# Optimization experiments

Hardware: AMD Instinct MI355X
Metric: run time of the kernel (lower is better)

Reference implementation:

```python
import jax, jax.numpy as jnp
import numpy as np

N_COARSE = 12500
N_FINE = 50000
MIN_BASIS = 16  # (min(L_in, L_out) + 1) ** 2 with L_in = L_out = 3


def setup_inputs() -> dict:
    key = jax.random.key(0)
    ks = jax.random.split(key, 8)
    return {
        "last_inv": jax.random.normal(ks[0], (N_COARSE, 256), dtype=jnp.float32),
        "cur_inv": jax.random.normal(ks[1], (N_FINE, 256), dtype=jnp.float32),
        "last_equ": jax.random.normal(ks[2], (N_COARSE, 16, 256), dtype=jnp.float32),
        "cur_equ": jax.random.normal(ks[3], (N_FINE, 16, 256), dtype=jnp.float32),
        "upsampling": jax.random.randint(ks[4], (N_FINE,), 0, N_COARSE, dtype=jnp.int32),
        # Linear weights stored as [in, out] (torch weight is [out, in]; x @ W.T == x @ W_in_out)
        "W_last_equ": jax.random.normal(ks[5], (256, 256), dtype=jnp.float32) * 0.02,
        "W_cur_equ": jax.random.normal(ks[6], (256, 256), dtype=jnp.float32) * 0.02,
        "W_mlp": jax.random.normal(ks[7], (768, 512), dtype=jnp.float32) * 0.02,
    }


def reference(last_inv, cur_inv, last_equ, cur_equ, upsampling, W_last_equ, W_cur_equ, W_mlp):
    # nearest_upsample: gather coarse rows up to fine resolution
    li = jnp.take(last_inv, upsampling, axis=0)                 # [N_fine, 256]
    le = jnp.take(last_equ, upsampling, axis=0)[:, :MIN_BASIS]  # [N_fine, 16, 256]
    le = jnp.einsum('nbc,cd->nbd', le, W_last_equ)              # fc_last_equ (no bias)
    ce = jnp.einsum('nbc,cd->nbd', cur_equ[:, :MIN_BASIS], W_cur_equ)  # fc_cur_equ
    equ = (ce * le).mean(axis=1)                                # [N_fine, 256]
    com = jnp.concatenate([li, cur_inv, equ], axis=-1)          # [N_fine, 768]
    return com @ W_mlp                                          # LastUnaryBlock: Linear, no bias
```

## Files before the change

kernel.cpp:

```cpp
#include <hip/hip_runtime.h>
#include <hip/hip_bf16.h>

#define N_COARSE 12500
#define N_FINE   50000

typedef __bf16 bf16x8 __attribute__((ext_vector_type(8)));
typedef __bf16 bf16x4 __attribute__((ext_vector_type(4)));
typedef float  f32x4  __attribute__((ext_vector_type(4)));


__device__ __forceinline__ bf16x8 cvt8(f32x4 x, f32x4 y) {
    bf16x8 r;
    r[0] = (__bf16)x[0]; r[1] = (__bf16)x[1]; r[2] = (__bf16)x[2]; r[3] = (__bf16)x[3];
    r[4] = (__bf16)y[0]; r[5] = (__bf16)y[1]; r[6] = (__bf16)y[2]; r[7] = (__bf16)y[3];
    return r;
}

__device__ __forceinline__ void lds_barrier() {
    asm volatile("s_waitcnt lgkmcnt(0)" ::: "memory");
    __builtin_amdgcn_s_barrier();
}

__device__ __forceinline__ void gl_lds16(const float* g, float* l) {
    __builtin_amdgcn_global_load_lds(
        (const __attribute__((address_space(1))) void*)g,
        (__attribute__((address_space(3))) void*)l, 16, 0, 0);
}

__device__ __forceinline__ int swz(int row, int byte) { return byte ^ ((row & 7) << 4); }
__device__ __forceinline__ void st_a(__bf16* lds, int row, int cs, bf16x8 v) {
    *(bf16x8*)((char*)lds + swz(row, row * 512 + cs * 16)) = v;
}
__device__ __forceinline__ bf16x8 ld_a(const __bf16* lds, int row, int ka) {
    return *(const bf16x8*)((const char*)lds + swz(row, row * 512 + ka * 2));
}

template<int NT>
__device__ __forceinline__ void stage_f32(const float* __restrict__ A, long row0,
                                          __bf16* lds, int tid, long maxrow) {
    const int r0 = tid >> 5, cs = tid & 31;
    constexpr int RPI = NT / 32;
    #pragma unroll
    for (int i = 0; i < 64 / RPI; ++i) {
        int row = r0 + i * RPI;
        long gr = row0 + row; if (gr > maxrow) gr = maxrow;
        const float* p = A + gr * 256 + cs * 8;
        f32x4 x = *(const f32x4*)p, y = *(const f32x4*)(p + 4);
        st_a(lds, row, cs, cvt8(x, y));
    }
}

__device__ __forceinline__ void mfma_tile(const __bf16* lds, const bf16x8* __restrict__ packB,
                                          int N, int c0, int ksb,
                                          f32x4 (&acc)[4][4], int lane) {
    const int g = lane >> 4, r15 = lane & 15;
    #pragma unroll
    for (int ks = 0; ks < 8; ++ks) {
        bf16x8 a[4];
        #pragma unroll
        for (int rt = 0; rt < 4; ++rt)
            a[rt] = ld_a(lds, rt * 16 + r15, ks * 32 + g * 8);
        const size_t kb = (size_t)((ksb + ks) * 4 + g) * N;
        #pragma unroll
        for (int ct = 0; ct < 4; ++ct) {
            bf16x8 b = packB[kb + c0 + ct * 16 + r15];
            #pragma unroll
            for (int rt = 0; rt < 4; ++rt)
                acc[rt][ct] = __builtin_amdgcn_mfma_f32_16x16x32_bf16(a[rt], b, acc[rt][ct], 0, 0, 0);
        }
    }
}

__global__ __launch_bounds__(256) void k_prep(
    const float* __restrict__ W_le, const float* __restrict__ W_ce,
    const float* __restrict__ W_mlp, const float* __restrict__ last_inv,
    __bf16* __restrict__ packLE, __bf16* __restrict__ packCE,
    __bf16* __restrict__ packM, __bf16* __restrict__ li_bf)
{
    const int b = blockIdx.x, tid = threadIdx.x;
    if (b < 256) {
        int idx = b * 256 + tid, k = idx >> 8, n = idx & 255;
        packLE[(((size_t)(k >> 3) << 8) + n) * 8 + (k & 7)] = (__bf16)W_le[idx];
    } else if (b < 512) {
        int idx = (b - 256) * 256 + tid, k = idx >> 8, n = idx & 255;
        packCE[(((size_t)(k >> 3) << 8) + n) * 8 + (k & 7)] = (__bf16)W_ce[idx];
    } else if (b < 2048) {
        int idx = (b - 512) * 256 + tid, k = idx >> 9, n = idx & 511;
        packM[(((size_t)(k >> 3) << 9) + n) * 8 + (k & 7)] = (__bf16)W_mlp[idx];
    } else {
        int i = (b - 2048) * 256 + tid;
        f32x4 v = ((const f32x4*)last_inv)[i];
        bf16x4 o;
        o[0] = (__bf16)v[0]; o[1] = (__bf16)v[1]; o[2] = (__bf16)v[2]; o[3] = (__bf16)v[3];
        ((bf16x4*)li_bf)[i] = o;
    }
}

__global__ __launch_bounds__(256) void k_coarse_equ(
    const float* __restrict__ last_equ, const bf16x8* __restrict__ packW,
    __bf16* __restrict__ LEp)
{
    __shared__ __attribute__((aligned(16))) float Af[2][32 * 256];
    const int tid = threadIdx.x, lane = tid & 63, wid = tid >> 6;
    const int g = lane >> 4, r15 = lane & 15;
    const int NT = N_COARSE * 16 / 32;
    const int per = (NT + gridDim.x - 1) / gridDim.x;
    const int tb = blockIdx.x * per;
    const int te = min(tb + per, NT);
    if (tb >= te) return;

    const int lhalf = (lane & 1) << 2;

    {
        const float* rb = last_equ + (size_t)tb * 32 * 256;
        #pragma unroll
        for (int i = 0; i < 8; ++i) {
            int row = wid * 8 + i;
            gl_lds16(rb + (size_t)row * 256 + ((((lane >> 1) ^ (row & 7)) << 3) + lhalf),
                     &Af[tb & 1][row * 256]);
        }
    }

    for (int t = tb; t < te; ++t) {
        asm volatile("s_waitcnt vmcnt(0)" ::: "memory");
        __builtin_amdgcn_s_barrier();

        if (t + 1 < te) {
            const float* rb = last_equ + (size_t)(t + 1) * 32 * 256;
            #pragma unroll
            for (int i = 0; i < 8; ++i) {
                int row = wid * 8 + i;
                gl_lds16(rb + (size_t)row * 256 + ((((lane >> 1) ^ (row & 7)) << 3) + lhalf),
                         &Af[(t + 1) & 1][row * 256]);
            }
        }

        const float* B = Af[t & 1];
        f32x4 acc[2][4] = {};
        #pragma unroll
        for (int ks = 0; ks < 8; ++ks) {
            bf16x8 a[2];
            #pragma unroll
            for (int rt = 0; rt < 2; ++rt) {
                int r = rt * 16 + r15;
                const float* p = B + r * 256 + (((4 * ks + g) ^ (r & 7)) << 3);
                a[rt] = cvt8(*(const f32x4*)p, *(const f32x4*)(p + 4));
            }
            const size_t kb = (size_t)(ks * 4 + g) * 256;
            #pragma unroll
            for (int ct = 0; ct < 4; ++ct) {
                bf16x8 b = packW[kb + wid * 64 + ct * 16 + r15];
                #pragma unroll
                for (int rt = 0; rt < 2; ++rt)
                    acc[rt][ct] = __builtin_amdgcn_mfma_f32_16x16x32_bf16(a[rt], b, acc[rt][ct], 0, 0, 0);
            }
        }

        #pragma unroll
        for (int rt = 0; rt < 2; ++rt) {
            int coarse = t * 2 + rt;
            #pragma unroll
            for (int ct = 0; ct < 4; ++ct) {
                int cg = wid * 4 + ct;
                bf16x4 v;
                v[0] = (__bf16)acc[rt][ct][0]; v[1] = (__bf16)acc[rt][ct][1];
                v[2] = (__bf16)acc[rt][ct][2]; v[3] = (__bf16)acc[rt][ct][3];
                *(bf16x4*)(LEp + ((size_t)(coarse * 16 + cg) * 64 + lane) * 4) = v;
            }
        }
    }
}

__global__ __launch_bounds__(256) void k_fine_equ(
    const float* __restrict__ cur_equ, const bf16x8* __restrict__ packW,
    const __bf16* __restrict__ LEp, const int* __restrict__ up,
    __bf16* __restrict__ equ)
{
    __shared__ __attribute__((aligned(16))) float Af[2][32 * 256];
    const int tid = threadIdx.x, lane = tid & 63, wid = tid >> 6;
    const int g = lane >> 4, r15 = lane & 15;
    const int NT = N_FINE / 2;
    const int per = (NT + gridDim.x - 1) / gridDim.x;
    const int tb = blockIdx.x * per;
    const int te = min(tb + per, NT);
    if (tb >= te) return;

    const int lhalf = (lane & 1) << 2;

    {
        const float* rb = cur_equ + (size_t)tb * 32 * 256;
        #pragma unroll
        for (int i = 0; i < 8; ++i) {
            int row = wid * 8 + i;
            gl_lds16(rb + (size_t)row * 256 + ((((lane >> 1) ^ (row & 7)) << 3) + lhalf),
                     &Af[tb & 1][row * 256]);
        }
    }

    for (int t = tb; t < te; ++t) {
        asm volatile("s_waitcnt vmcnt(0)" ::: "memory");
        __builtin_amdgcn_s_barrier();

        if (t + 1 < te) {
            const float* rb = cur_equ + (size_t)(t + 1) * 32 * 256;
            #pragma unroll
            for (int i = 0; i < 8; ++i) {
                int row = wid * 8 + i;
                gl_lds16(rb + (size_t)row * 256 + ((((lane >> 1) ^ (row & 7)) << 3) + lhalf),
                         &Af[(t + 1) & 1][row * 256]);
            }
        }

        const float* B = Af[t & 1];
        f32x4 acc[2][4] = {};
        #pragma unroll
        for (int ks = 0; ks < 8; ++ks) {
            bf16x8 a[2];
            #pragma unroll
            for (int rt = 0; rt < 2; ++rt) {
                int r = rt * 16 + r15;
                const float* p = B + r * 256 + (((4 * ks + g) ^ (r & 7)) << 3);
                a[rt] = cvt8(*(const f32x4*)p, *(const f32x4*)(p + 4));
            }
            const size_t kb = (size_t)(ks * 4 + g) * 256;
            #pragma unroll
            for (int ct = 0; ct < 4; ++ct) {
                bf16x8 b = packW[kb + wid * 64 + ct * 16 + r15];
                #pragma unroll
                for (int rt = 0; rt < 2; ++rt)
                    acc[rt][ct] = __builtin_amdgcn_mfma_f32_16x16x32_bf16(a[rt], b, acc[rt][ct], 0, 0, 0);
            }
        }

        const int n0 = t * 2;
        const int cu0 = up[n0], cu1 = up[n0 + 1];
        bf16x4 le[2][4];
        #pragma unroll
        for (int ct = 0; ct < 4; ++ct) {
            le[0][ct] = *(const bf16x4*)(LEp + ((size_t)(cu0 * 16 + wid * 4 + ct) * 64 + lane) * 4);
            le[1][ct] = *(const bf16x4*)(LEp + ((size_t)(cu1 * 16 + wid * 4 + ct) * 64 + lane) * 4);
        }
        #pragma unroll
        for (int rt = 0; rt < 2; ++rt) {
            #pragma unroll
            for (int ct = 0; ct < 4; ++ct) {
                float s = acc[rt][ct][0] * (float)le[rt][ct][0]
                        + acc[rt][ct][1] * (float)le[rt][ct][1]
                        + acc[rt][ct][2] * (float)le[rt][ct][2]
                        + acc[rt][ct][3] * (float)le[rt][ct][3];
                s += __shfl_xor(s, 16, 64);
                s += __shfl_xor(s, 32, 64);
                if (lane < 16)
                    equ[(size_t)(n0 + rt) * 256 + wid * 64 + ct * 16 + lane] =
                        (__bf16)(s * 0.0625f);
            }
        }
    }
}

__global__ __launch_bounds__(512) void k_out(
    const __bf16* __restrict__ li_bf, const float* __restrict__ cur_inv,
    const __bf16* __restrict__ equ, const bf16x8* __restrict__ packW,
    const int* __restrict__ up, float* __restrict__ out)
{
    __shared__ __attribute__((aligned(16))) __bf16 As[64 * 256];
    const int tid = threadIdx.x, lane = tid & 63, wid = tid >> 6;
    const int row0 = blockIdx.x * 64;
    const int c0 = wid * 64;
    const int r0 = tid >> 5, cs = tid & 31;
    f32x4 acc[4][4] = {};

    #pragma unroll
    for (int i = 0; i < 4; ++i) {
        int row = r0 + i * 16;
        int gr = row0 + row; if (gr > N_FINE - 1) gr = N_FINE - 1;
        st_a(As, row, cs, *(const bf16x8*)(li_bf + (size_t)up[gr] * 256 + cs * 8));
    }
    lds_barrier();
    mfma_tile(As, packW, 512, c0, 0, acc, lane);
    lds_barrier();

    stage_f32<512>(cur_inv, row0, As, tid, N_FINE - 1);
    lds_barrier();
    mfma_tile(As, packW, 512, c0, 8, acc, lane);
    lds_barrier();

    #pragma unroll
    for (int i = 0; i < 4; ++i) {
        int row = r0 + i * 16;
        int gr = row0 + row; if (gr > N_FINE - 1) gr = N_FINE - 1;
        st_a(As, row, cs, *(const bf16x8*)(equ + (size_t)gr * 256 + cs * 8));
    }
    lds_barrier();
    mfma_tile(As, packW, 512, c0, 16, acc, lane);

    const int g = lane >> 4, r15 = lane & 15;
    #pragma unroll
    for (int rt = 0; rt < 4; ++rt)
        #pragma unroll
        for (int j = 0; j < 4; ++j) {
            int r = row0 + rt * 16 + g * 4 + j;
            if (r < N_FINE)
                #pragma unroll
                for (int ct = 0; ct < 4; ++ct)
                    out[(size_t)r * 512 + c0 + ct * 16 + r15] = acc[rt][ct][j];
        }
}

extern "C" void kernel_launch(void* const* d_in, const int* in_sizes, int n_in,
                              void* d_out, int out_size, void* d_ws, size_t ws_size,
                              hipStream_t stream) {
    const float* last_inv = (const float*)d_in[0];
    const float* cur_inv  = (const float*)d_in[1];
    const float* last_equ = (const float*)d_in[2];
    const float* cur_equ  = (const float*)d_in[3];
    const int*   up       = (const int*)d_in[4];
    const float* W_le     = (const float*)d_in[5];
    const float* W_ce     = (const float*)d_in[6];
    const float* W_mlp    = (const float*)d_in[7];
    float* out = (float*)d_out;

    char* w = (char*)d_ws;
    __bf16* LEp    = (__bf16*)w;  w += (size_t)N_COARSE * 16 * 256 * 2;
    __bf16* equ    = (__bf16*)w;  w += (size_t)N_FINE * 256 * 2;
    __bf16* li_bf  = (__bf16*)w;  w += (size_t)N_COARSE * 256 * 2;
    __bf16* packLE = (__bf16*)w;  w += (size_t)256 * 256 * 2;
    __bf16* packCE = (__bf16*)w;  w += (size_t)256 * 256 * 2;
    __bf16* packM  = (__bf16*)w;  w += (size_t)768 * 512 * 2;

    k_prep<<<2048 + 3125, 256, 0, stream>>>(
        W_le, W_ce, W_mlp, last_inv, packLE, packCE, packM, li_bf);

    k_coarse_equ<<<512, 256, 0, stream>>>(
        last_equ, (const bf16x8*)packLE, LEp);

    k_fine_equ<<<512, 256, 0, stream>>>(
        cur_equ, (const bf16x8*)packCE, LEp, up, equ);

    k_out<<<(N_FINE + 63) / 64, 512, 0, stream>>>(
        li_bf, cur_inv, equ, (const bf16x8*)packM, up, out);
}
```

Before: 483.4 us.

## Double-buffer k_out A-tiles with async global-to-LDS loads and pre-convert cur_inv

Moves the fp32-to-bf16 conversion of cur_inv into the prep kernel, so the output GEMM reads a bf16 copy. k_out now stages each A segment straight into LDS with global_load_lds into two buffers, so the next segment's load overlaps MFMA on the current one. The aim is to hide load latency in k_out and drop the register round-trip. The cost is an extra full pass writing and reading a 25.6MB bf16 copy of cur_inv, plus double the LDS per block, which may lower occupancy.

```diff
diff --git a/kernel.cpp b/kernel.cpp
--- a/kernel.cpp
+++ b/kernel.cpp
@@ -16,38 +16,15 @@
     return r;
 }
 
-__device__ __forceinline__ void lds_barrier() {
-    asm volatile("s_waitcnt lgkmcnt(0)" ::: "memory");
-    __builtin_amdgcn_s_barrier();
-}
-
-__device__ __forceinline__ void gl_lds16(const float* g, float* l) {
+__device__ __forceinline__ void gl_lds16(const void* g, void* l) {
     __builtin_amdgcn_global_load_lds(
         (const __attribute__((address_space(1))) void*)g,
         (__attribute__((address_space(3))) void*)l, 16, 0, 0);
 }
 
 __device__ __forceinline__ int swz(int row, int byte) { return byte ^ ((row & 7) << 4); }
-__device__ __forceinline__ void st_a(__bf16* lds, int row, int cs, bf16x8 v) {
-    *(bf16x8*)((char*)lds + swz(row, row * 512 + cs * 16)) = v;
-}
 __device__ __forceinline__ bf16x8 ld_a(const __bf16* lds, int row, int ka) {
     return *(const bf16x8*)((const char*)lds + swz(row, row * 512 + ka * 2));
-}
-
-template<int NT>
-__device__ __forceinline__ void stage_f32(const float* __restrict__ A, long row0,
-                                          __bf16* lds, int tid, long maxrow) {
-    const int r0 = tid >> 5, cs = tid & 31;
-    constexpr int RPI = NT / 32;
-    #pragma unroll
-    for (int i = 0; i < 64 / RPI; ++i) {
-        int row = r0 + i * RPI;
-        long gr = row0 + row; if (gr > maxrow) gr = maxrow;
-        const float* p = A + gr * 256 + cs * 8;
-        f32x4 x = *(const f32x4*)p, y = *(const f32x4*)(p + 4);
-        st_a(lds, row, cs, cvt8(x, y));
-    }
 }
 
 __device__ __forceinline__ void mfma_tile(const __bf16* lds, const bf16x8* __restrict__ packB,
@@ -74,8 +51,10 @@
 __global__ __launch_bounds__(256) void k_prep(
     const float* __restrict__ W_le, const float* __restrict__ W_ce,
     const float* __restrict__ W_mlp, const float* __restrict__ last_inv,
+    const float* __restrict__ cur_inv,
     __bf16* __restrict__ packLE, __bf16* __restrict__ packCE,
-    __bf16* __restrict__ packM, __bf16* __restrict__ li_bf)
+    __bf16* __restrict__ packM, __bf16* __restrict__ li_bf,
+    __bf16* __restrict__ ci_bf)
 {
     const int b = blockIdx.x, tid = threadIdx.x;
     if (b < 256) {
@@ -87,12 +66,18 @@
     } else if (b < 2048) {
         int idx = (b - 512) * 256 + tid, k = idx >> 9, n = idx & 511;
         packM[(((size_t)(k >> 3) << 9) + n) * 8 + (k & 7)] = (__bf16)W_mlp[idx];
-    } else {
+    } else if (b < 2048 + 3125) {
         int i = (b - 2048) * 256 + tid;
         f32x4 v = ((const f32x4*)last_inv)[i];
         bf16x4 o;
         o[0] = (__bf16)v[0]; o[1] = (__bf16)v[1]; o[2] = (__bf16)v[2]; o[3] = (__bf16)v[3];
         ((bf16x4*)li_bf)[i] = o;
+    } else {
+        int i = (b - 2048 - 3125) * 256 + tid;
+        f32x4 v = ((const f32x4*)cur_inv)[i];
+        bf16x4 o;
+        o[0] = (__bf16)v[0]; o[1] = (__bf16)v[1]; o[2] = (__bf16)v[2]; o[3] = (__bf16)v[3];
+        ((bf16x4*)ci_bf)[i] = o;
     }
 }
 
@@ -110,7 +95,6 @@
     if (tb >= te) return;
 
     const int lhalf = (lane & 1) << 2;
-
     {
         const float* rb = last_equ + (size_t)tb * 32 * 256;
         #pragma unroll
@@ -186,7 +170,6 @@
     if (tb >= te) return;
 
     const int lhalf = (lane & 1) << 2;
-
     {
         const float* rb = cur_equ + (size_t)tb * 32 * 256;
         #pragma unroll
@@ -259,40 +242,54 @@
 }
 
 __global__ __launch_bounds__(512) void k_out(
-    const __bf16* __restrict__ li_bf, const float* __restrict__ cur_inv,
+    const __bf16* __restrict__ li_bf, const __bf16* __restrict__ ci_bf,
     const __bf16* __restrict__ equ, const bf16x8* __restrict__ packW,
     const int* __restrict__ up, float* __restrict__ out)
 {
-    __shared__ __attribute__((aligned(16))) __bf16 As[64 * 256];
-    const int tid = threadIdx.x, lane = tid & 63, wid = tid >> 6;
+    __shared__ __attribute__((aligned(16))) __bf16 Ab[2][64 * 256];
+    const int tid = threadIdx.x, lane = tid & 63;
+    const int c0 = (tid >> 6) * 64;
     const int row0 = blockIdx.x * 64;
-    const int c0 = wid * 64;
-    const int r0 = tid >> 5, cs = tid & 31;
+    const int wbase = (tid >> 6) * 2;
+
+    #pragma unroll
+    for (int i = 0; i < 4; ++i) {
+        int rw = (tid >> 5) + i * 16;
+        int gr = row0 + rw; if (gr > N_FINE - 1) gr = N_FINE - 1;
+        int gran = (tid & 31) ^ (rw & 7);
+        gl_lds16(li_bf + (size_t)up[gr] * 256 + gran * 8,
+                 &Ab[0][(wbase + i * 16) * 256]);
+    }
+
     f32x4 acc[4][4] = {};
 
+    asm volatile("s_waitcnt vmcnt(0)" ::: "memory");
+    __builtin_amdgcn_s_barrier();
     #pragma unroll
     for (int i = 0; i < 4; ++i) {
-        int row = r0 + i * 16;
-        int gr = row0 + row; if (gr > N_FINE - 1) gr = N_FINE - 1;
-        st_a(As, row, cs, *(const bf16x8*)(li_bf + (size_t)up[gr] * 256 + cs * 8));
-    }
-    lds_barrier();
-    mfma_tile(As, packW, 512, c0, 0, acc, lane);
-    lds_barrier();
-
-    stage_f32<512>(cur_inv, row0, As, tid, N_FINE - 1);
-    lds_barrier();
-    mfma_tile(As, packW, 512, c0, 8, acc, lane);
-    lds_barrier();
-
+        int rw = (tid >> 5) + i * 16;
+        int gr = row0 + rw; if (gr > N_FINE - 1) gr = N_FINE - 1;
+        int gran = (tid & 31) ^ (rw & 7);
+        gl_lds16(ci_bf + (size_t)gr * 256 + gran * 8,
+                 &Ab[1][(wbase + i * 16) * 256]);
+    }
+    mfma_tile(Ab[0], packW, 512, c0, 0, acc, lane);
+
+    asm volatile("s_waitcnt vmcnt(0)" ::: "memory");
+    __builtin_amdgcn_s_barrier();
     #pragma unroll
     for (int i = 0; i < 4; ++i) {
-        int row = r0 + i * 16;
-        int gr = row0 + row; if (gr > N_FINE - 1) gr = N_FINE - 1;
-        st_a(As, row, cs, *(const bf16x8*)(equ + (size_t)gr * 256 + cs * 8));
-    }
-    lds_barrier();
-    mfma_tile(As, packW, 512, c0, 16, acc, lane);
+        int rw = (tid >> 5) + i * 16;
+        int gr = row0 + rw; if (gr > N_FINE - 1) gr = N_FINE - 1;
+        int gran = (tid & 31) ^ (rw & 7);
+        gl_lds16(equ + (size_t)gr * 256 + gran * 8,
+                 &Ab[0][(wbase + i * 16) * 256]);
+    }
+    mfma_tile(Ab[1], packW, 512, c0, 8, acc, lane);
+
+    asm volatile("s_waitcnt vmcnt(0)" ::: "memory");
+    __builtin_amdgcn_s_barrier();
+    mfma_tile(Ab[0], packW, 512, c0, 16, acc, lane);
 
     const int g = lane >> 4, r15 = lane & 15;
     #pragma unroll
@@ -324,12 +321,13 @@
     __bf16* LEp    = (__bf16*)w;  w += (size_t)N_COARSE * 16 * 256 * 2;
     __bf16* equ    = (__bf16*)w;  w += (size_t)N_FINE * 256 * 2;
     __bf16* li_bf  = (__bf16*)w;  w += (size_t)N_COARSE * 256 * 2;
+    __bf16* ci_bf  = (__bf16*)w;  w += (size_t)N_FINE * 256 * 2;
     __bf16* packLE = (__bf16*)w;  w += (size_t)256 * 256 * 2;
     __bf16* packCE = (__bf16*)w;  w += (size_t)256 * 256 * 2;
     __bf16* packM  = (__bf16*)w;  w += (size_t)768 * 512 * 2;
 
-    k_prep<<<2048 + 3125, 256, 0, stream>>>(
-        W_le, W_ce, W_mlp, last_inv, packLE, packCE, packM, li_bf);
+    k_prep<<<2048 + 3125 + 12500, 256, 0, stream>>>(
+        W_le, W_ce, W_mlp, last_inv, cur_inv, packLE, packCE, packM, li_bf, ci_bf);
 
     k_coarse_equ<<<512, 256, 0, stream>>>(
         last_equ, (const bf16x8*)packLE, LEp);
@@ -338,5 +336,5 @@
         cur_equ, (const bf16x8*)packCE, LEp, up, equ);
 
     k_out<<<(N_FINE + 63) / 64, 512, 0, stream>>>(
-        li_bf, cur_inv, equ, (const bf16x8*)packM, up, out);
-}
+        li_bf, ci_bf, equ, (const bf16x8*)packM, up, out);
+}
```

Measured after the change: 493.8 us. 1.02x slower.
